# Kernel tuning notes

Hardware: AMD Instinct MI355X
Metric: run time of the kernel (lower is better)

The kernel has to match this reference:

```python
import jax, jax.numpy as jnp
import numpy as np

N_NODES = 100000
N_EDGES = 1600000
IN_DIM, HID, OUT = 128, 64, 64
KERNEL = 5
PAD = (KERNEL - 1) // 2


def setup_inputs() -> dict:
    key = jax.random.key(0)
    ks = jax.random.split(key, 12)
    s = lambda fan_in: 1.0 / np.sqrt(fan_in)
    return {
        "x": jax.random.normal(ks[0], (N_NODES, IN_DIM), jnp.float32),
        "edge_index": jax.random.randint(ks[1], (2, N_EDGES), 0, N_NODES, jnp.int32),
        "W0": jax.random.normal(ks[2], (IN_DIM, HID), jnp.float32) * s(IN_DIM),
        "b0": jnp.zeros((HID,), jnp.float32),
        "W1": jax.random.normal(ks[3], (HID, HID), jnp.float32) * s(HID),
        "b1": jnp.zeros((HID,), jnp.float32),
        "W2": jax.random.normal(ks[4], (HID, OUT), jnp.float32) * s(HID),
        "b2": jnp.zeros((OUT,), jnp.float32),
        "Wp": jax.random.normal(ks[5], (OUT, 1), jnp.float32) * s(OUT),
        "bp": jnp.zeros((1,), jnp.float32),
        "conv1_w": jax.random.normal(ks[6], (OUT, OUT, KERNEL), jnp.float32) * s(OUT * KERNEL),
        "conv1_b": jnp.zeros((OUT,), jnp.float32),
        "conv2_w": jax.random.normal(ks[7], (OUT, OUT, KERNEL), jnp.float32) * s(OUT * KERNEL),
        "conv2_b": jnp.zeros((OUT,), jnp.float32),
        "lin_w": jax.random.normal(ks[8], (2 * OUT, OUT), jnp.float32) * s(2 * OUT),
        "lin_b": jnp.zeros((OUT,), jnp.float32),
    }


def gcn_conv(h, W, b, src, dst, n):
    """PyG GCNConv: x @ W, add self-loops, D^-1/2 (A+I) D^-1/2 aggregation, + bias."""
    h = h @ W  # [N, out]
    loop = jnp.arange(n, dtype=src.dtype)
    srcl = jnp.concatenate([src, loop])
    dstl = jnp.concatenate([dst, loop])
    deg = jax.ops.segment_sum(jnp.ones_like(dstl, dtype=h.dtype), dstl, num_segments=n)
    dinv = jnp.where(deg > 0, jax.lax.rsqrt(deg), 0.0)
    norm = dinv[srcl] * dinv[dstl]  # [E+N]
    out = jax.ops.segment_sum(h[srcl] * norm[:, None], dstl, num_segments=n)
    return out + b


def conv1d(x, w, b):
    # x: [1, C, N], w: [Cout, Cin, K]
    y = jax.lax.conv_general_dilated(x, w, window_strides=(1,), padding=[(PAD, PAD)],
                                     dimension_numbers=("NCH", "OIH", "NCH"))
    return y + b[None, :, None]


def reference(x, edge_index, W0, b0, W1, b1, W2, b2, Wp, bp,
              conv1_w, conv1_b, conv2_w, conv2_b, lin_w, lin_b):
    n = x.shape[0]
    src, dst = edge_index[0], edge_index[1]
    # eval mode: dropout layers are identity
    h = jax.nn.relu(gcn_conv(x, W0, b0, src, dst, n))
    h = jax.nn.relu(gcn_conv(h, W1, b1, src, dst, n))
    h1 = gcn_conv(h, W2, b2, src, dst, n)  # [N, OUT]
    g_score = h1 @ Wp + bp  # [N, 1]
    sorted_idx = jnp.argsort(g_score[:, 0])  # ascending, as torch.sort
    inverse_idx = jnp.argsort(sorted_idx)
    sorted_x = g_score[sorted_idx] * h1[sorted_idx]  # [N, OUT]
    sorted_x = sorted_x.T[None]  # [1, OUT, N]
    sorted_x = jax.nn.relu(conv1d(sorted_x, conv1_w, conv1_b))
    sorted_x = conv1d(sorted_x, conv2_w, conv2_b)
    sorted_x = sorted_x[0].T  # [N, OUT]
    h2 = sorted_x[inverse_idx]  # un-sort back to node order
    out = jnp.concatenate([h1, h2], axis=1) @ lin_w + lin_b  # [N, OUT]
    return out
```

## Files before the change

kernel.cpp:

```cpp
#include <hip/hip_runtime.h>

#define NN 100000
#define NE 1600000
#define NB_SCAN 98
#define RBLK 98
#define NENT (256 * RBLK)
#define RSEG 25

__global__ void zero_counts(int* c) {
    int i = blockIdx.x * blockDim.x + threadIdx.x;
    if (i < NN) c[i] = 0;
}

__global__ void count_dst(const int* __restrict__ dst, int* c) {
    int e = blockIdx.x * blockDim.x + threadIdx.x;
    if (e < NE) atomicAdd(&c[dst[e]], 1);
}

__global__ void scan_p1(const int* __restrict__ c, int* __restrict__ bsums) {
    __shared__ int red[256];
    int b = blockIdx.x, t = threadIdx.x;
    int s = 0;
    for (int i = t; i < 1024; i += 256) {
        int idx = b * 1024 + i;
        s += (idx < NN) ? c[idx] : 0;
    }
    red[t] = s; __syncthreads();
    for (int o = 128; o; o >>= 1) {
        if (t < o) red[t] += red[t + o];
        __syncthreads();
    }
    if (t == 0) bsums[b] = red[0];
}

__global__ void scan_p2(int* bsums) {
    __shared__ int tmp[128];
    int t = threadIdx.x;
    int v = (t < NB_SCAN) ? bsums[t] : 0;
    tmp[t] = v; __syncthreads();
    for (int o = 1; o < 128; o <<= 1) {
        int add = (t >= o) ? tmp[t - o] : 0;
        __syncthreads();
        tmp[t] += add;
        __syncthreads();
    }
    if (t < NB_SCAN) bsums[t] = tmp[t] - v;
}

__global__ void scan_p3(const int* __restrict__ c, const int* __restrict__ bsums,
                        int* __restrict__ offs, int* __restrict__ cursor,
                        float* __restrict__ dinv) {
    __shared__ int thr[256];
    int b = blockIdx.x, t = threadIdx.x;
    int base = b * 1024 + t * 4;
    int cv[4];
#pragma unroll
    for (int j = 0; j < 4; j++) cv[j] = (base + j < NN) ? c[base + j] : 0;
    int s = cv[0] + cv[1] + cv[2] + cv[3];
    thr[t] = s; __syncthreads();
    for (int o = 1; o < 256; o <<= 1) {
        int add = (t >= o) ? thr[t - o] : 0;
        __syncthreads();
        thr[t] += add;
        __syncthreads();
    }
    int ex = thr[t] - s + bsums[b];
#pragma unroll
    for (int j = 0; j < 4; j++) {
        if (base + j < NN) {
            offs[base + j] = ex;
            cursor[base + j] = ex;
            dinv[base + j] = rsqrtf((float)(cv[j] + 1));
            ex += cv[j];
        }
    }
}

__global__ void csr_scatter(const int* __restrict__ src, const int* __restrict__ dst,
                            int* cursor, int* __restrict__ csr) {
    int e = blockIdx.x * blockDim.x + threadIdx.x;
    if (e >= NE) return;
    int p = atomicAdd(&cursor[dst[e]], 1);
    csr[p] = src[e];
}

__device__ inline void swz_w(const float* __restrict__ W, float4* __restrict__ o, int idx) {
    int k4 = idx >> 6, co = idx & 63;
    o[idx] = make_float4(W[(4 * k4 + 0) * 64 + co], W[(4 * k4 + 1) * 64 + co],
                         W[(4 * k4 + 2) * 64 + co], W[(4 * k4 + 3) * 64 + co]);
}

__device__ inline void swz_c(const float* __restrict__ w, float4* __restrict__ o, int idx) {
    int co = idx & 63, j = (idx >> 6) & 15, k = idx >> 10;
    int b = co * 320 + k;
    o[idx] = make_float4(w[b + (4 * j + 0) * 5], w[b + (4 * j + 1) * 5],
                         w[b + (4 * j + 2) * 5], w[b + (4 * j + 3) * 5]);
}

__global__ void swizzle_all(const float* W0, const float* W1, const float* W2,
                            const float* lw, const float* c1w, const float* c2w,
                            float4* w0sw, float4* w1sw, float4* w2sw,
                            float4* linsw, float4* c1sw, float4* c2sw) {
    int idx = blockIdx.x * blockDim.x + threadIdx.x;
    if (idx < 2048)        swz_w(W0, w0sw, idx);
    else if (idx < 3072)   swz_w(W1, w1sw, idx - 2048);
    else if (idx < 4096)   swz_w(W2, w2sw, idx - 3072);
    else if (idx < 6144)   swz_w(lw, linsw, idx - 4096);
    else if (idx < 11264)  swz_c(c1w, c1sw, idx - 6144);
    else if (idx < 16384)  swz_c(c2w, c2sw, idx - 11264);
}

template <int K, bool RELU>
__global__ __launch_bounds__(256) void gemm64r(const float* __restrict__ X,
                                               const float4* __restrict__ Wsw,
                                               const float* __restrict__ dinv,
                                               float* __restrict__ Y, int n) {
    constexpr int KV = K / 4;
    constexpr int SH = (KV == 32) ? 5 : 4;
    __shared__ float4 xs[64][KV];
    int tid = threadIdx.x;
    int r0 = blockIdx.x * 64;
    for (int idx = tid; idx < 64 * KV; idx += 256) {
        int r = idx >> SH, k4 = idx & (KV - 1);
        int row = r0 + r;
        float4 v = make_float4(0.f, 0.f, 0.f, 0.f);
        if (row < n) v = *reinterpret_cast<const float4*>(X + (size_t)row * K + 4 * k4);
        if (RELU) {
            v.x = fmaxf(v.x, 0.f); v.y = fmaxf(v.y, 0.f);
            v.z = fmaxf(v.z, 0.f); v.w = fmaxf(v.w, 0.f);
        }
        xs[r][k4] = v;
    }
    __syncthreads();
    int co2 = tid & 31, rg = tid >> 5;
    int c0 = 2 * co2;
    float acc0[8], acc1[8];
#pragma unroll
    for (int i = 0; i < 8; i++) { acc0[i] = 0.f; acc1[i] = 0.f; }
    for (int k4 = 0; k4 < KV; k4++) {
        float4 wa = Wsw[k4 * 64 + c0];
        float4 wb = Wsw[k4 * 64 + c0 + 1];
#pragma unroll
        for (int i = 0; i < 8; i++) {
            float4 xv = xs[rg * 8 + i][k4];
            acc0[i] += xv.x * wa.x + xv.y * wa.y + xv.z * wa.z + xv.w * wa.w;
            acc1[i] += xv.x * wb.x + xv.y * wb.y + xv.z * wb.z + xv.w * wb.w;
        }
    }
#pragma unroll
    for (int i = 0; i < 8; i++) {
        int row = r0 + rg * 8 + i;
        if (row < n) {
            float dv = dinv[row];
            *reinterpret_cast<float2*>(Y + (size_t)row * 64 + c0) =
                make_float2(acc0[i] * dv, acc1[i] * dv);
        }
    }
}

template <int SCORE>
__global__ __launch_bounds__(256) void agg_pull(const float* __restrict__ H,
                                                const int* __restrict__ offs,
                                                const int* __restrict__ counts,
                                                const int* __restrict__ csr,
                                                const float* __restrict__ dinv,
                                                const float* __restrict__ bias,
                                                float* __restrict__ Y,
                                                const float* __restrict__ Wp,
                                                const float* __restrict__ bp,
                                                float* __restrict__ sc,
                                                unsigned* __restrict__ keys,
                                                int* __restrict__ vals) {
    int lane = threadIdx.x & 63;
    int node = blockIdx.x * 4 + (threadIdx.x >> 6);
    if (node >= NN) return;
    float dv = dinv[node];
    float acc = H[(size_t)node * 64 + lane];
    int off = offs[node], cnt = counts[node];
    int i = 0;
    for (; i + 7 < cnt; i += 8) {
        int p0 = csr[off + i];
        int p1 = csr[off + i + 1];
        int p2 = csr[off + i + 2];
        int p3 = csr[off + i + 3];
        int p4 = csr[off + i + 4];
        int p5 = csr[off + i + 5];
        int p6 = csr[off + i + 6];
        int p7 = csr[off + i + 7];
        float h0 = H[(size_t)p0 * 64 + lane];
        float h1 = H[(size_t)p1 * 64 + lane];
        float h2 = H[(size_t)p2 * 64 + lane];
        float h3 = H[(size_t)p3 * 64 + lane];
        float h4 = H[(size_t)p4 * 64 + lane];
        float h5 = H[(size_t)p5 * 64 + lane];
        float h6 = H[(size_t)p6 * 64 + lane];
        float h7 = H[(size_t)p7 * 64 + lane];
        acc += ((h0 + h1) + (h2 + h3)) + ((h4 + h5) + (h6 + h7));
    }
    for (; i < cnt; i++) {
        acc += H[(size_t)csr[off + i] * 64 + lane];
    }
    float o = acc * dv + bias[lane];
    Y[(size_t)node * 64 + lane] = o;
    if (SCORE) {
        float v = o * Wp[lane];
        for (int of = 32; of; of >>= 1) v += __shfl_down(v, of, 64);
        if (lane == 0) {
            float s = v + bp[0];
            sc[node] = s;
            unsigned u = __float_as_uint(s);
            u = (u & 0x80000000u) ? ~u : (u | 0x80000000u);
            keys[node] = u;
            vals[node] = node;
        }
    }
}

__global__ __launch_bounds__(256) void radix_hist(const unsigned* __restrict__ keys,
                                                  int* __restrict__ hist, int shift) {
    __shared__ int h[256];
    int t = threadIdx.x;
    h[t] = 0;
    __syncthreads();
    int base = blockIdx.x * 1024;
    for (int i = t; i < 1024; i += 256) {
        int idx = base + i;
        if (idx < NN) atomicAdd(&h[(keys[idx] >> shift) & 255], 1);
    }
    __syncthreads();
    hist[t * RBLK + blockIdx.x] = h[t];
}

__global__ __launch_bounds__(1024) void radix_scan(int* hist) {
    __shared__ int partial[1024];
    int t = threadIdx.x;
    int base = t * RSEG;
    int loc[RSEG];
    int s = 0;
#pragma unroll
    for (int i = 0; i < RSEG; i++) {
        int idx = base + i;
        int v = (idx < NENT) ? hist[idx] : 0;
        loc[i] = s;
        s += v;
    }
    partial[t] = s;
    __syncthreads();
    for (int o = 1; o < 1024; o <<= 1) {
        int add = (t >= o) ? partial[t - o] : 0;
        __syncthreads();
        partial[t] += add;
        __syncthreads();
    }
    int ex = partial[t] - s;
#pragma unroll
    for (int i = 0; i < RSEG; i++) {
        int idx = base + i;
        if (idx < NENT) hist[idx] = ex + loc[i];
    }
}

__global__ __launch_bounds__(256) void radix_scatter(const unsigned* __restrict__ keys_in,
                                                     const int* __restrict__ vals_in,
                                                     const int* __restrict__ hist,
                                                     unsigned* __restrict__ keys_out,
                                                     int* __restrict__ vals_out, int shift) {
    __shared__ int cursor[256];
    __shared__ int whist[4][256];
    __shared__ int wbase[4][256];
    int t = threadIdx.x, w = t >> 6, lane = t & 63;
    cursor[t] = hist[t * RBLK + blockIdx.x];
    __syncthreads();
    int base = blockIdx.x * 1024;
    for (int r = 0; r < 4; r++) {
        int idx = base + r * 256 + t;
        bool active = idx < NN;
        unsigned key = 0;
        int val = 0, d = -1;
        if (active) {
            key = keys_in[idx];
            val = vals_in[idx];
            d = (key >> shift) & 255;
        }
#pragma unroll
        for (int q = 0; q < 4; q++) whist[q][t] = 0;
        __syncthreads();
        unsigned long long m = __ballot(active);
#pragma unroll
        for (int b = 0; b < 8; b++) {
            unsigned long long bb = __ballot(active && ((d >> b) & 1));
            m &= ((d >> b) & 1) ? bb : ~bb;
        }
        unsigned long long below = ((unsigned long long)1 << lane) - 1;
        int rank_in_wave = __popcll(m & below);
        int cnt_in_wave = __popcll(m);
        if (active && rank_in_wave == 0) whist[w][d] = cnt_in_wave;
        __syncthreads();
        int c0 = whist[0][t], c1 = whist[1][t], c2 = whist[2][t], c3 = whist[3][t];
        wbase[0][t] = 0;
        wbase[1][t] = c0;
        wbase[2][t] = c0 + c1;
        wbase[3][t] = c0 + c1 + c2;
        __syncthreads();
        if (active) {
            int pos = cursor[d] + wbase[w][d] + rank_in_wave;
            keys_out[pos] = key;
            vals_out[pos] = val;
        }
        __syncthreads();
        cursor[t] += c0 + c1 + c2 + c3;
    }
}

template <bool GATHER>
__global__ __launch_bounds__(256) void conv1d_k(const float* __restrict__ X,
                                                const int* __restrict__ vals,
                                                const float* __restrict__ sc,
                                                const float4* __restrict__ cw,
                                                const float* __restrict__ bias,
                                                float* __restrict__ Y, int relu,
                                                int* __restrict__ inv) {
    __shared__ float4 xs[68][16];
    int tid = threadIdx.x;
    int r0 = blockIdx.x * 64;
    for (int idx = tid; idx < 68 * 16; idx += 256) {
        int r = idx >> 4, k4 = idx & 15;
        int row = r0 + r - 2;
        float4 v = make_float4(0.f, 0.f, 0.f, 0.f);
        if (row >= 0 && row < NN) {
            if (GATHER) {
                int vs = vals[row];
                float s = sc[vs];
                v = *reinterpret_cast<const float4*>(X + (size_t)vs * 64 + 4 * k4);
                v.x *= s; v.y *= s; v.z *= s; v.w *= s;
                if (k4 == 0) inv[vs] = row;
            } else {
                v = *reinterpret_cast<const float4*>(X + (size_t)row * 64 + 4 * k4);
            }
        }
        xs[r][k4] = v;
    }
    __syncthreads();
    int co2 = tid & 31, rg = tid >> 5;
    int c0 = 2 * co2;
    float acc0[8], acc1[8];
#pragma unroll
    for (int i = 0; i < 8; i++) { acc0[i] = 0.f; acc1[i] = 0.f; }
    for (int j = 0; j < 16; j++) {
        float4 xv[12];
#pragma unroll
        for (int t2 = 0; t2 < 12; t2++) xv[t2] = xs[rg * 8 + t2][j];
#pragma unroll
        for (int k = 0; k < 5; k++) {
            float4 wa = cw[(k * 16 + j) * 64 + c0];
            float4 wb = cw[(k * 16 + j) * 64 + c0 + 1];
#pragma unroll
            for (int i = 0; i < 8; i++) {
                float4 x4 = xv[i + k];
                acc0[i] += x4.x * wa.x + x4.y * wa.y + x4.z * wa.z + x4.w * wa.w;
                acc1[i] += x4.x * wb.x + x4.y * wb.y + x4.z * wb.z + x4.w * wb.w;
            }
        }
    }
    float b0v = bias[c0], b1v = bias[c0 + 1];
#pragma unroll
    for (int i = 0; i < 8; i++) {
        int row = r0 + rg * 8 + i;
        if (row < NN) {
            float o0 = acc0[i] + b0v, o1 = acc1[i] + b1v;
            if (relu) { o0 = fmaxf(o0, 0.f); o1 = fmaxf(o1, 0.f); }
            *reinterpret_cast<float2*>(Y + (size_t)row * 64 + c0) = make_float2(o0, o1);
        }
    }
}

__global__ __launch_bounds__(256) void final_k(const float* __restrict__ C,
                                               const float* __restrict__ H2,
                                               const int* __restrict__ inv,
                                               const float4* __restrict__ linsw,
                                               const float* __restrict__ lb,
                                               float* __restrict__ Yout) {
    __shared__ float4 xs[64][32];
    int tid = threadIdx.x;
    int r0 = blockIdx.x * 64;
    for (int idx = tid; idx < 64 * 32; idx += 256) {
        int r = idx >> 5, k4 = idx & 31;
        int row = r0 + r;
        float4 v = make_float4(0.f, 0.f, 0.f, 0.f);
        if (row < NN) {
            if (k4 < 16) v = *reinterpret_cast<const float4*>(C + (size_t)row * 64 + 4 * k4);
            else v = *reinterpret_cast<const float4*>(H2 + (size_t)inv[row] * 64 + 4 * (k4 - 16));
        }
        xs[r][k4] = v;
    }
    __syncthreads();
    int co2 = tid & 31, rg = tid >> 5;
    int c0 = 2 * co2;
    float acc0[8], acc1[8];
#pragma unroll
    for (int i = 0; i < 8; i++) { acc0[i] = 0.f; acc1[i] = 0.f; }
    for (int k4 = 0; k4 < 32; k4++) {
        float4 wa = linsw[k4 * 64 + c0];
        float4 wb = linsw[k4 * 64 + c0 + 1];
#pragma unroll
        for (int i = 0; i < 8; i++) {
            float4 xv = xs[rg * 8 + i][k4];
            acc0[i] += xv.x * wa.x + xv.y * wa.y + xv.z * wa.z + xv.w * wa.w;
            acc1[i] += xv.x * wb.x + xv.y * wb.y + xv.z * wb.z + xv.w * wb.w;
        }
    }
    float b0v = lb[c0], b1v = lb[c0 + 1];
#pragma unroll
    for (int i = 0; i < 8; i++) {
        int row = r0 + rg * 8 + i;
        if (row < NN)
            *reinterpret_cast<float2*>(Yout + (size_t)row * 64 + c0) =
                make_float2(acc0[i] + b0v, acc1[i] + b1v);
    }
}

extern "C" void kernel_launch(void* const* d_in, const int* in_sizes, int n_in,
                              void* d_out, int out_size, void* d_ws, size_t ws_size,
                              hipStream_t stream) {
    const float* x   = (const float*)d_in[0];
    const int*   ei  = (const int*)d_in[1];
    const float* W0  = (const float*)d_in[2];
    const float* b0  = (const float*)d_in[3];
    const float* W1  = (const float*)d_in[4];
    const float* b1  = (const float*)d_in[5];
    const float* W2  = (const float*)d_in[6];
    const float* b2  = (const float*)d_in[7];
    const float* Wp  = (const float*)d_in[8];
    const float* bp  = (const float*)d_in[9];
    const float* c1w = (const float*)d_in[10];
    const float* c1b = (const float*)d_in[11];
    const float* c2w = (const float*)d_in[12];
    const float* c2b = (const float*)d_in[13];
    const float* lw  = (const float*)d_in[14];
    const float* lb  = (const float*)d_in[15];
    const int* src = ei;
    const int* dst = ei + NE;

    const int NNP = 100352;
    float* A     = (float*)d_ws;
    float* B     = A + (size_t)NN * 64;
    float* dinv  = B + (size_t)NN * 64;
    float* score = dinv + NNP;
    unsigned* keys0 = (unsigned*)(score + NNP);
    int* vals0   = (int*)(keys0 + NNP);
    unsigned* keys1 = (unsigned*)(vals0 + NNP);
    int* vals1   = (int*)(keys1 + NNP);
    int* rhist   = vals1 + NNP;
    int* inv     = rhist + NENT;
    int* counts  = inv + NNP;
    int* offs    = counts + NNP;
    int* cursor  = offs + NNP;
    int* bsums   = cursor + NNP;
    int* csr     = bsums + 128;
    float4* w0sw  = (float4*)(csr + NE);
    float4* w1sw  = w0sw + 2048;
    float4* w2sw  = w1sw + 1024;
    float4* linsw = w2sw + 1024;
    float4* c1sw  = linsw + 2048;
    float4* c2sw  = c1sw + 5120;
    float* Cb = (float*)d_out;

    const int GR64 = (NN + 63) / 64;
    const int GN4 = (NN + 3) / 4;
    const int GE = (NE + 255) / 256;

    zero_counts<<<(NN + 255) / 256, 256, 0, stream>>>(counts);
    count_dst<<<GE, 256, 0, stream>>>(dst, counts);
    scan_p1<<<NB_SCAN, 256, 0, stream>>>(counts, bsums);
    scan_p2<<<1, 128, 0, stream>>>(bsums);
    scan_p3<<<NB_SCAN, 256, 0, stream>>>(counts, bsums, offs, cursor, dinv);
    csr_scatter<<<GE, 256, 0, stream>>>(src, dst, cursor, csr);

    swizzle_all<<<64, 256, 0, stream>>>(W0, W1, W2, lw, c1w, c2w,
                                        w0sw, w1sw, w2sw, linsw, c1sw, c2sw);

    gemm64r<128, false><<<GR64, 256, 0, stream>>>(x, w0sw, dinv, A, NN);
    agg_pull<0><<<GN4, 256, 0, stream>>>(A, offs, counts, csr, dinv, b0, B,
                                         nullptr, nullptr, nullptr, nullptr, nullptr);
    gemm64r<64, true><<<GR64, 256, 0, stream>>>(B, w1sw, dinv, A, NN);
    agg_pull<0><<<GN4, 256, 0, stream>>>(A, offs, counts, csr, dinv, b1, B,
                                         nullptr, nullptr, nullptr, nullptr, nullptr);
    gemm64r<64, true><<<GR64, 256, 0, stream>>>(B, w2sw, dinv, A, NN);
    agg_pull<1><<<GN4, 256, 0, stream>>>(A, offs, counts, csr, dinv, b2, Cb,
                                         Wp, bp, score, keys0, vals0);

    radix_hist<<<RBLK, 256, 0, stream>>>(keys0, rhist, 0);
    radix_scan<<<1, 1024, 0, stream>>>(rhist);
    radix_scatter<<<RBLK, 256, 0, stream>>>(keys0, vals0, rhist, keys1, vals1, 0);
    radix_hist<<<RBLK, 256, 0, stream>>>(keys1, rhist, 8);
    radix_scan<<<1, 1024, 0, stream>>>(rhist);
    radix_scatter<<<RBLK, 256, 0, stream>>>(keys1, vals1, rhist, keys0, vals0, 8);
    radix_hist<<<RBLK, 256, 0, stream>>>(keys0, rhist, 16);
    radix_scan<<<1, 1024, 0, stream>>>(rhist);
    radix_scatter<<<RBLK, 256, 0, stream>>>(keys0, vals0, rhist, keys1, vals1, 16);
    radix_hist<<<RBLK, 256, 0, stream>>>(keys1, rhist, 24);
    radix_scan<<<1, 1024, 0, stream>>>(rhist);
    radix_scatter<<<RBLK, 256, 0, stream>>>(keys1, vals1, rhist, keys0, vals0, 24);

    conv1d_k<true><<<GR64, 256, 0, stream>>>(Cb, vals0, score, c1sw, c1b, B, 1, inv);
    conv1d_k<false><<<GR64, 256, 0, stream>>>(B, nullptr, nullptr, c2sw, c2b, A, 0, nullptr);

    final_k<<<GR64, 256, 0, stream>>>(Cb, A, inv, linsw, lb, (float*)d_out);
}
```

Measured before the change: 924.0 us.

## Build CSR via two-level bucket sort instead of global atomic counting sort

Replaces per-edge global atomics for degree counting and CSR scatter with a bucketed counting sort. Edges are first grouped into 256-node buckets using shared-memory histograms and packed src/low-dst words in a staging buffer. Each bucket is then placed into CSR by one block with shared-memory atomics, which also produces offsets, counts and dinv. This aims to cut random global atomic traffic and scattered writes, at the cost of an extra pass over the edges and a staging buffer. Packing src<<8 relies on node ids fitting in 24 bits.

```diff
diff --git a/kernel.cpp b/kernel.cpp
--- a/kernel.cpp
+++ b/kernel.cpp
@@ -2,86 +2,117 @@
 
 #define NN 100000
 #define NE 1600000
-#define NB_SCAN 98
+#define NBUK 391
 #define RBLK 98
 #define NENT (256 * RBLK)
 #define RSEG 25
-
-__global__ void zero_counts(int* c) {
+#define BS_CHUNK 8192
+#define NBS 196
+
+__global__ void zero_bhist(int* bhist) {
     int i = blockIdx.x * blockDim.x + threadIdx.x;
-    if (i < NN) c[i] = 0;
-}
-
-__global__ void count_dst(const int* __restrict__ dst, int* c) {
-    int e = blockIdx.x * blockDim.x + threadIdx.x;
-    if (e < NE) atomicAdd(&c[dst[e]], 1);
-}
-
-__global__ void scan_p1(const int* __restrict__ c, int* __restrict__ bsums) {
-    __shared__ int red[256];
+    if (i < NBUK) bhist[i] = 0;
+}
+
+__global__ __launch_bounds__(256) void bucket_hist(const int* __restrict__ dst, int* __restrict__ bhist) {
+    __shared__ int h[NBUK];
+    int t = threadIdx.x;
+    for (int b = t; b < NBUK; b += 256) h[b] = 0;
+    __syncthreads();
+    int base = blockIdx.x * BS_CHUNK;
+    for (int i = t; i < BS_CHUNK; i += 256) {
+        int e = base + i;
+        if (e < NE) atomicAdd(&h[dst[e] >> 8], 1);
+    }
+    __syncthreads();
+    for (int b = t; b < NBUK; b += 256)
+        if (h[b]) atomicAdd(&bhist[b], h[b]);
+}
+
+__global__ __launch_bounds__(512) void bucket_scan(const int* __restrict__ bhist,
+                                                   int* __restrict__ bbase, int* __restrict__ bcur) {
+    __shared__ int tmp[512];
+    int t = threadIdx.x;
+    int v = (t < NBUK) ? bhist[t] : 0;
+    tmp[t] = v; __syncthreads();
+    for (int o = 1; o < 512; o <<= 1) {
+        int add = (t >= o) ? tmp[t - o] : 0;
+        __syncthreads();
+        tmp[t] += add;
+        __syncthreads();
+    }
+    int ex = tmp[t] - v;
+    if (t < NBUK) { bbase[t] = ex; bcur[t] = ex; }
+    if (t == NBUK - 1) bbase[NBUK] = ex + v;
+}
+
+__global__ __launch_bounds__(256) void bucket_scatter(const int* __restrict__ src,
+                                                      const int* __restrict__ dst,
+                                                      int* __restrict__ bcur,
+                                                      unsigned* __restrict__ stage) {
+    __shared__ int h[NBUK];
+    int t = threadIdx.x;
+    for (int b = t; b < NBUK; b += 256) h[b] = 0;
+    __syncthreads();
+    int base = blockIdx.x * BS_CHUNK;
+    for (int i = t; i < BS_CHUNK; i += 256) {
+        int e = base + i;
+        if (e < NE) atomicAdd(&h[dst[e] >> 8], 1);
+    }
+    __syncthreads();
+    for (int b = t; b < NBUK; b += 256) {
+        int c = h[b];
+        h[b] = c ? atomicAdd(&bcur[b], c) : 0;
+    }
+    __syncthreads();
+    for (int i = t; i < BS_CHUNK; i += 256) {
+        int e = base + i;
+        if (e < NE) {
+            int d = dst[e];
+            int p = atomicAdd(&h[d >> 8], 1);
+            stage[p] = ((unsigned)src[e] << 8) | (unsigned)(d & 255);
+        }
+    }
+}
+
+__global__ __launch_bounds__(256) void csr_place(const unsigned* __restrict__ stage,
+                                                 const int* __restrict__ bbase,
+                                                 int* __restrict__ csr,
+                                                 int* __restrict__ counts,
+                                                 int* __restrict__ offs,
+                                                 float* __restrict__ dinv) {
+    __shared__ int cnt[256];
+    __shared__ int cursor[256];
     int b = blockIdx.x, t = threadIdx.x;
-    int s = 0;
-    for (int i = t; i < 1024; i += 256) {
-        int idx = b * 1024 + i;
-        s += (idx < NN) ? c[idx] : 0;
-    }
-    red[t] = s; __syncthreads();
-    for (int o = 128; o; o >>= 1) {
-        if (t < o) red[t] += red[t + o];
-        __syncthreads();
-    }
-    if (t == 0) bsums[b] = red[0];
-}
-
-__global__ void scan_p2(int* bsums) {
-    __shared__ int tmp[128];
-    int t = threadIdx.x;
-    int v = (t < NB_SCAN) ? bsums[t] : 0;
-    tmp[t] = v; __syncthreads();
-    for (int o = 1; o < 128; o <<= 1) {
+    int start = bbase[b], end = bbase[b + 1];
+    cnt[t] = 0;
+    __syncthreads();
+    for (int idx = start + t; idx < end; idx += 256)
+        atomicAdd(&cnt[stage[idx] & 255u], 1);
+    __syncthreads();
+    int c = cnt[t];
+    __shared__ int tmp[256];
+    tmp[t] = c; __syncthreads();
+    for (int o = 1; o < 256; o <<= 1) {
         int add = (t >= o) ? tmp[t - o] : 0;
         __syncthreads();
         tmp[t] += add;
         __syncthreads();
     }
-    if (t < NB_SCAN) bsums[t] = tmp[t] - v;
-}
-
-__global__ void scan_p3(const int* __restrict__ c, const int* __restrict__ bsums,
-                        int* __restrict__ offs, int* __restrict__ cursor,
-                        float* __restrict__ dinv) {
-    __shared__ int thr[256];
-    int b = blockIdx.x, t = threadIdx.x;
-    int base = b * 1024 + t * 4;
-    int cv[4];
-#pragma unroll
-    for (int j = 0; j < 4; j++) cv[j] = (base + j < NN) ? c[base + j] : 0;
-    int s = cv[0] + cv[1] + cv[2] + cv[3];
-    thr[t] = s; __syncthreads();
-    for (int o = 1; o < 256; o <<= 1) {
-        int add = (t >= o) ? thr[t - o] : 0;
-        __syncthreads();
-        thr[t] += add;
-        __syncthreads();
-    }
-    int ex = thr[t] - s + bsums[b];
-#pragma unroll
-    for (int j = 0; j < 4; j++) {
-        if (base + j < NN) {
-            offs[base + j] = ex;
-            cursor[base + j] = ex;
-            dinv[base + j] = rsqrtf((float)(cv[j] + 1));
-            ex += cv[j];
-        }
-    }
-}
-
-__global__ void csr_scatter(const int* __restrict__ src, const int* __restrict__ dst,
-                            int* cursor, int* __restrict__ csr) {
-    int e = blockIdx.x * blockDim.x + threadIdx.x;
-    if (e >= NE) return;
-    int p = atomicAdd(&cursor[dst[e]], 1);
-    csr[p] = src[e];
+    int pos = start + tmp[t] - c;
+    cursor[t] = pos;
+    int node = b * 256 + t;
+    if (node < NN) {
+        offs[node] = pos;
+        counts[node] = c;
+        dinv[node] = rsqrtf((float)(c + 1));
+    }
+    __syncthreads();
+    for (int idx = start + t; idx < end; idx += 256) {
+        unsigned u = stage[idx];
+        int p = atomicAdd(&cursor[u & 255u], 1);
+        csr[p] = (int)(u >> 8);
+    }
 }
 
 __device__ inline void swz_w(const float* __restrict__ W, float4* __restrict__ o, int idx) {
@@ -454,9 +485,11 @@
     int* inv     = rhist + NENT;
     int* counts  = inv + NNP;
     int* offs    = counts + NNP;
-    int* cursor  = offs + NNP;
-    int* bsums   = cursor + NNP;
-    int* csr     = bsums + 128;
+    int* bhist   = offs + NNP;
+    int* bbase   = bhist + 512;
+    int* bcur    = bbase + 512;
+    unsigned* stage = (unsigned*)(bcur + 512);
+    int* csr     = (int*)(stage + NE);
     float4* w0sw  = (float4*)(csr + NE);
     float4* w1sw  = w0sw + 2048;
     float4* w2sw  = w1sw + 1024;
@@ -467,14 +500,12 @@
 
     const int GR64 = (NN + 63) / 64;
     const int GN4 = (NN + 3) / 4;
-    const int GE = (NE + 255) / 256;
-
-    zero_counts<<<(NN + 255) / 256, 256, 0, stream>>>(counts);
-    count_dst<<<GE, 256, 0, stream>>>(dst, counts);
-    scan_p1<<<NB_SCAN, 256, 0, stream>>>(counts, bsums);
-    scan_p2<<<1, 128, 0, stream>>>(bsums);
-    scan_p3<<<NB_SCAN, 256, 0, stream>>>(counts, bsums, offs, cursor, dinv);
-    csr_scatter<<<GE, 256, 0, stream>>>(src, dst, cursor, csr);
+
+    zero_bhist<<<2, 256, 0, stream>>>(bhist);
+    bucket_hist<<<NBS, 256, 0, stream>>>(dst, bhist);
+    bucket_scan<<<1, 512, 0, stream>>>(bhist, bbase, bcur);
+    bucket_scatter<<<NBS, 256, 0, stream>>>(src, dst, bcur, stage);
+    csr_place<<<NBUK, 256, 0, stream>>>(stage, bbase, csr, counts, offs, dinv);
 
     swizzle_all<<<64, 256, 0, stream>>>(W0, W1, W2, lw, c1w, c2w,
                                         w0sw, w1sw, w2sw, linsw, c1sw, c2sw);
```

Result: faster. 783.9 us (-15.2%).
